# Optimization experiments

Hardware: AMD Instinct MI355X
Metric: run time of the kernel (lower is better)

Reference implementation:

```python
import jax, jax.numpy as jnp
import numpy as np

B, T, F, H, C = 32, 512, 512, 1024, 1000


def setup_inputs() -> dict:
    key = jax.random.key(0)
    ks = jax.random.split(key, 9)
    return {
        "data": jax.random.normal(ks[0], (B, T, F), dtype=jnp.float32),
        "h0": jax.random.normal(ks[1], (H,), dtype=jnp.float32),
        "c0": jax.random.normal(ks[2], (H,), dtype=jnp.float32),
        "w_f": jax.random.normal(ks[3], (H + F, H), dtype=jnp.float32),
        "w_i": jax.random.normal(ks[4], (H + F, H), dtype=jnp.float32),
        "w_c1": jax.random.normal(ks[5], (H + F, H), dtype=jnp.float32),
        "w_o": jax.random.normal(ks[6], (H + F, H), dtype=jnp.float32),
        "fc_w": jax.random.normal(ks[7], (C, H), dtype=jnp.float32),
        "fc_b": jax.random.normal(ks[8], (C,), dtype=jnp.float32),
    }


def reference(data, h0, c0, w_f, w_i, w_c1, w_o, fc_w, fc_b):
    b, t, _ = data.shape
    h = h0.shape[0]
    # Original module never updates h0/c0 inside the time loop, so every
    # timestep sees the same initial state; vectorize gates over time.
    z = jnp.concatenate([jnp.broadcast_to(h0, (b, t, h)), data], axis=-1)  # [B,T,H+F]
    # Stack the 4 gate weights into one fused matmul: [H+F, 4H]
    w_all = jnp.concatenate([w_f, w_i, w_c1, w_o], axis=1)
    g = jnp.einsum('btz,zk->btk', z, w_all)  # [B,T,4H]
    f_g, i_g, c1_g, o_g = jnp.split(g, 4, axis=-1)
    f_g = jax.nn.sigmoid(f_g)
    i_g = jax.nn.sigmoid(i_g)
    c1_g = jnp.tanh(c1_g)
    o_g = jax.nn.sigmoid(o_g)
    c = f_g * c0 + i_g * c1_g          # [B,T,H]
    h_all = o_g * jnp.tanh(c)          # [B,T,H]
    h_last = h_all[:, -1]              # output depends on last timestep only
    logits = jax.nn.relu(h_last @ fc_w.T + fc_b)
    return jax.nn.log_softmax(logits, axis=1)
```

## Files before the change

### kernel.cpp

```cpp
#include <hip/hip_runtime.h>
#include <math.h>

#define BB 32
#define TT 512
#define FF 512
#define HH 1024
#define CC 1000
#define QQ (4*HH)
#define FCB 8
#define KCN 4

template<int JCH, int CHH, int JCD, int CHD>
__global__ __launch_bounds__(512, 4) void k_gates(
    const float* __restrict__ data, const float* __restrict__ h0,
    const float* __restrict__ wf, const float* __restrict__ wi,
    const float* __restrict__ wc, const float* __restrict__ wo,
    float* __restrict__ hp, float* __restrict__ dp)
{
    constexpr int LDSN = (BB*JCD > JCH) ? BB*JCD : JCH;
    __shared__ float lds[LDSN];
    const int t  = threadIdx.x;
    const int bx = blockIdx.x;
    constexpr int NH0 = 2*CHH;

    if (bx < NH0) {
        const int cb2 = bx & 1;
        const int ch  = bx >> 1;
        const int q   = cb2*2048 + t*4;
        const int gate = q >> 10;
        const int k4   = q & (HH-1);
        const float* w = (gate==0) ? wf : (gate==1) ? wi : (gate==2) ? wc : wo;
        if (t < JCH) lds[t] = h0[ch*JCH + t];
        __syncthreads();
        float4 s = make_float4(0.f,0.f,0.f,0.f);
        #pragma unroll
        for (int j = 0; j < JCH; j += 4) {
            const float4 w0 = *(const float4*)(w + (size_t)(ch*JCH + j+0)*HH + k4);
            const float4 w1 = *(const float4*)(w + (size_t)(ch*JCH + j+1)*HH + k4);
            const float4 w2 = *(const float4*)(w + (size_t)(ch*JCH + j+2)*HH + k4);
            const float4 w3 = *(const float4*)(w + (size_t)(ch*JCH + j+3)*HH + k4);
            const float h0v = lds[j+0], h1v = lds[j+1], h2v = lds[j+2], h3v = lds[j+3];
            s.x += h0v*w0.x; s.y += h0v*w0.y; s.z += h0v*w0.z; s.w += h0v*w0.w;
            s.x += h1v*w1.x; s.y += h1v*w1.y; s.z += h1v*w1.z; s.w += h1v*w1.w;
            s.x += h2v*w2.x; s.y += h2v*w2.y; s.z += h2v*w2.z; s.w += h2v*w2.w;
            s.x += h3v*w3.x; s.y += h3v*w3.y; s.z += h3v*w3.z; s.w += h3v*w3.w;
        }
        *(float4*)(hp + (size_t)ch*QQ + q) = s;
    } else {
        const int idx  = bx - NH0;
        const int cb   = idx & 15;
        const int cd   = idx >> 4;
        const int q0   = cb*256;
        const int gate = q0 >> 10;
        const int k0   = q0 & (HH-1);
        const float* w = (gate==0) ? wf : (gate==1) ? wi : (gate==2) ? wc : wo;
        const int jc0  = cd*JCD;

        constexpr int SL = BB*JCD/4;
        for (int s = t; s < SL; s += 512) {
            const int b  = s / (JCD/4);
            const int jj = (s % (JCD/4))*4;
            const float4 v = *(const float4*)(data + (size_t)b*TT*FF + (size_t)(TT-1)*FF + jc0 + jj);
            lds[b*JCD + jj+0] = v.x; lds[b*JCD + jj+1] = v.y;
            lds[b*JCD + jj+2] = v.z; lds[b*JCD + jj+3] = v.w;
        }
        __syncthreads();

        const int c4 = t & 63;
        const int b0 = (t >> 6) * 4;
        const int k4 = k0 + c4*4;
        float4 acc[4];
        #pragma unroll
        for (int bi = 0; bi < 4; ++bi) acc[bi] = make_float4(0.f,0.f,0.f,0.f);

        #pragma unroll 2
        for (int j = 0; j < JCD; j += 4) {
            const float4 w0 = *(const float4*)(w + (size_t)(HH + jc0 + j+0)*HH + k4);
            const float4 w1 = *(const float4*)(w + (size_t)(HH + jc0 + j+1)*HH + k4);
            const float4 w2 = *(const float4*)(w + (size_t)(HH + jc0 + j+2)*HH + k4);
            const float4 w3 = *(const float4*)(w + (size_t)(HH + jc0 + j+3)*HH + k4);
            #pragma unroll
            for (int bi = 0; bi < 4; ++bi) {
                const float d0 = lds[(b0+bi)*JCD + j+0];
                const float d1 = lds[(b0+bi)*JCD + j+1];
                const float d2 = lds[(b0+bi)*JCD + j+2];
                const float d3 = lds[(b0+bi)*JCD + j+3];
                acc[bi].x += d0*w0.x; acc[bi].y += d0*w0.y; acc[bi].z += d0*w0.z; acc[bi].w += d0*w0.w;
                acc[bi].x += d1*w1.x; acc[bi].y += d1*w1.y; acc[bi].z += d1*w1.z; acc[bi].w += d1*w1.w;
                acc[bi].x += d2*w2.x; acc[bi].y += d2*w2.y; acc[bi].z += d2*w2.z; acc[bi].w += d2*w2.w;
                acc[bi].x += d3*w3.x; acc[bi].y += d3*w3.y; acc[bi].z += d3*w3.z; acc[bi].w += d3*w3.w;
            }
        }
        #pragma unroll
        for (int bi = 0; bi < 4; ++bi)
            *(float4*)(dp + ((size_t)cd*BB + b0 + bi)*QQ + q0 + c4*4) = acc[bi];
    }
}

template<int CH, int CD>
__global__ __launch_bounds__(256, 2) void k_cell(
    const float* __restrict__ hp, const float* __restrict__ dp,
    const float* __restrict__ c0, float* __restrict__ hlast)
{
    __shared__ float4 p[4][64];
    const int t    = threadIdx.x;
    const int kblk = blockIdx.x;
    const int b    = blockIdx.y;
    const int g    = t >> 6;
    const int i    = t & 63;
    const int q    = g*HH + kblk*256 + i*4;

    float4 s = make_float4(0.f,0.f,0.f,0.f);
    #pragma unroll 8
    for (int ch = 0; ch < CH; ++ch) {
        const float4 v = *(const float4*)(hp + (size_t)ch*QQ + q);
        s.x += v.x; s.y += v.y; s.z += v.z; s.w += v.w;
    }
    #pragma unroll 8
    for (int cd = 0; cd < CD; ++cd) {
        const float4 v = *(const float4*)(dp + ((size_t)cd*BB + b)*QQ + q);
        s.x += v.x; s.y += v.y; s.z += v.z; s.w += v.w;
    }
    p[g][i] = s;
    __syncthreads();

    if (t < 64) {
        const float4 gf = p[0][t], gi = p[1][t], gc = p[2][t], go = p[3][t];
        const float4 cv = *(const float4*)(c0 + kblk*256 + t*4);
        float4 h;
        {
            const float f = 1.f/(1.f + expf(-gf.x)), ii = 1.f/(1.f + expf(-gi.x));
            const float cg = tanhf(gc.x), o = 1.f/(1.f + expf(-go.x));
            h.x = o*tanhf(f*cv.x + ii*cg);
        }
        {
            const float f = 1.f/(1.f + expf(-gf.y)), ii = 1.f/(1.f + expf(-gi.y));
            const float cg = tanhf(gc.y), o = 1.f/(1.f + expf(-go.y));
            h.y = o*tanhf(f*cv.y + ii*cg);
        }
        {
            const float f = 1.f/(1.f + expf(-gf.z)), ii = 1.f/(1.f + expf(-gi.z));
            const float cg = tanhf(gc.z), o = 1.f/(1.f + expf(-go.z));
            h.z = o*tanhf(f*cv.z + ii*cg);
        }
        {
            const float f = 1.f/(1.f + expf(-gf.w)), ii = 1.f/(1.f + expf(-gi.w));
            const float cg = tanhf(gc.w), o = 1.f/(1.f + expf(-go.w));
            h.w = o*tanhf(f*cv.w + ii*cg);
        }
        *(float4*)(hlast + (size_t)b*HH + kblk*256 + t*4) = h;
    }
}

__global__ __launch_bounds__(256) void k_fc_part(
    const float* __restrict__ hlast, const float* __restrict__ fcw,
    float* __restrict__ pl)
{
    __shared__ float hs[BB][257];
    __shared__ float wl[FCB][257];
    const int t  = threadIdx.x;
    const int c0 = blockIdx.x * FCB;
    const int kc = blockIdx.y;
    const int k0 = kc*256;
    const int b  = t & 31;
    const int cl = t >> 5;
    const int c  = c0 + cl;

    for (int l = t; l < BB*64; l += 256) {
        const int bb = l >> 6, kk = l & 63;
        const float4 v = *(const float4*)(hlast + (size_t)bb*HH + k0 + kk*4);
        hs[bb][kk*4+0] = v.x; hs[bb][kk*4+1] = v.y;
        hs[bb][kk*4+2] = v.z; hs[bb][kk*4+3] = v.w;
    }
    for (int l = t; l < FCB*64; l += 256) {
        const int cc = l >> 6, kk = l & 63;
        const float4 v = *(const float4*)(fcw + (size_t)(c0+cc)*HH + k0 + kk*4);
        wl[cc][kk*4+0] = v.x; wl[cc][kk*4+1] = v.y;
        wl[cc][kk*4+2] = v.z; wl[cc][kk*4+3] = v.w;
    }
    __syncthreads();

    float acc = 0.f;
    #pragma unroll 16
    for (int k = 0; k < 256; ++k)
        acc += hs[b][k] * wl[cl][k];
    pl[((size_t)kc*BB + b)*CC + c] = acc;
}

__global__ __launch_bounds__(256) void k_lsm(
    const float* __restrict__ pl, const float* __restrict__ fcb,
    float* __restrict__ out)
{
    __shared__ float red[8];
    const int b = blockIdx.x, t = threadIdx.x;
    float v[4]; float vmax = -1e30f;
    #pragma unroll
    for (int ci = 0; ci < 4; ++ci) {
        const int c = t + ci*256;
        if (c < CC) {
            float s = pl[((size_t)0*BB + b)*CC + c]
                    + pl[((size_t)1*BB + b)*CC + c]
                    + pl[((size_t)2*BB + b)*CC + c]
                    + pl[((size_t)3*BB + b)*CC + c]
                    + fcb[c];
            v[ci] = fmaxf(s, 0.f);
            vmax = fmaxf(vmax, v[ci]);
        } else v[ci] = -1e30f;
    }
    for (int o = 32; o > 0; o >>= 1) vmax = fmaxf(vmax, __shfl_down(vmax, o, 64));
    const int lane = t & 63, wid = t >> 6;
    if (lane == 0) red[wid] = vmax;
    __syncthreads();
    if (t == 0) red[4] = fmaxf(fmaxf(red[0], red[1]), fmaxf(red[2], red[3]));
    __syncthreads();
    const float m = red[4];
    float se = 0.f;
    #pragma unroll
    for (int ci = 0; ci < 4; ++ci) {
        const int c = t + ci*256;
        if (c < CC) se += expf(v[ci] - m);
    }
    for (int o = 32; o > 0; o >>= 1) se += __shfl_down(se, o, 64);
    if (lane == 0) red[wid] = se;
    __syncthreads();
    if (t == 0) red[5] = m + logf(red[0] + red[1] + red[2] + red[3]);
    __syncthreads();
    const float lse = red[5];
    #pragma unroll
    for (int ci = 0; ci < 4; ++ci) {
        const int c = t + ci*256;
        if (c < CC) out[(size_t)b*CC + c] = v[ci] - lse;
    }
}

extern "C" void kernel_launch(void* const* d_in, const int* in_sizes, int n_in,
                              void* d_out, int out_size, void* d_ws, size_t ws_size,
                              hipStream_t stream) {
    const float* data = (const float*)d_in[0];
    const float* h0   = (const float*)d_in[1];
    const float* c0   = (const float*)d_in[2];
    const float* wf   = (const float*)d_in[3];
    const float* wi   = (const float*)d_in[4];
    const float* wc   = (const float*)d_in[5];
    const float* wo   = (const float*)d_in[6];
    const float* fcw  = (const float*)d_in[7];
    const float* fcb  = (const float*)d_in[8];
    float* out = (float*)d_out;

    const size_t needA = ((size_t)32*QQ + (size_t)16*BB*QQ + (size_t)BB*HH + (size_t)KCN*BB*CC) * 4;
    const bool cfgA = (ws_size >= needA);

    float* ws = (float*)d_ws;
    if (cfgA) {
        float* hp = ws;
        float* dp = hp + (size_t)32*QQ;
        float* hl = dp + (size_t)16*BB*QQ;
        float* pl = hl + (size_t)BB*HH;
        k_gates<32,32,32,16><<<dim3(2*32 + 16*16), 512, 0, stream>>>(data, h0, wf, wi, wc, wo, hp, dp);
        k_cell<32,16><<<dim3(HH/256, BB), 256, 0, stream>>>(hp, dp, c0, hl);
        k_fc_part<<<dim3(CC/FCB, KCN), 256, 0, stream>>>(hl, fcw, pl);
        k_lsm<<<dim3(BB), 256, 0, stream>>>(pl, fcb, out);
    } else {
        float* hp = ws;
        float* dp = hp + (size_t)32*QQ;
        float* hl = dp + (size_t)4*BB*QQ;
        float* pl = hl + (size_t)BB*HH;
        k_gates<32,32,128,4><<<dim3(2*32 + 16*4), 512, 0, stream>>>(data, h0, wf, wi, wc, wo, hp, dp);
        k_cell<32,4><<<dim3(HH/256, BB), 256, 0, stream>>>(hp, dp, c0, hl);
        k_fc_part<<<dim3(CC/FCB, KCN), 256, 0, stream>>>(hl, fcw, pl);
        k_lsm<<<dim3(BB), 256, 0, stream>>>(pl, fcb, out);
    }
}
```

Before: 31.70 us.

## Fuse four LSTM-head kernels into one persistent kernel with grid barriers

```diff
diff --git a/kernel.cpp b/kernel.cpp
--- a/kernel.cpp
+++ b/kernel.cpp
@@ -9,6 +9,247 @@
 #define QQ (4*HH)
 #define FCB 8
 #define KCN 4
+
+#define NBLK 320
+#define PJCH 32
+#define PCHH 32
+#define PJCD 32
+#define PCHD 16
+
+__device__ __forceinline__ void gbar(int* cnt) {
+    __syncthreads();
+    if (threadIdx.x == 0) {
+        __threadfence();
+        atomicAdd(cnt, 1);
+        while (atomicAdd(cnt, 0) < NBLK) __builtin_amdgcn_s_sleep(2);
+        __threadfence();
+    }
+    __syncthreads();
+}
+
+__global__ __launch_bounds__(512, 4) void k_fused(
+    const float* __restrict__ data, const float* __restrict__ h0,
+    const float* __restrict__ c0,
+    const float* __restrict__ wf, const float* __restrict__ wi,
+    const float* __restrict__ wc, const float* __restrict__ wo,
+    const float* __restrict__ fcw, const float* __restrict__ fcb,
+    float* __restrict__ hp, float* __restrict__ dp,
+    float* __restrict__ hl, float* __restrict__ pl,
+    float* __restrict__ out, int* __restrict__ bars)
+{
+    __shared__ __align__(16) float smem[48*257];
+    const int t   = threadIdx.x;
+    const int blk = blockIdx.x;
+
+    if (blk < 2*PCHH) {
+        const int cb2 = blk & 1;
+        const int ch  = blk >> 1;
+        const int q   = cb2*2048 + t*4;
+        const int gate = q >> 10;
+        const int k4   = q & (HH-1);
+        const float* w = (gate==0) ? wf : (gate==1) ? wi : (gate==2) ? wc : wo;
+        if (t < PJCH) smem[t] = h0[ch*PJCH + t];
+        __syncthreads();
+        float4 s = make_float4(0.f,0.f,0.f,0.f);
+        #pragma unroll
+        for (int j = 0; j < PJCH; j += 4) {
+            const float4 w0 = *(const float4*)(w + (size_t)(ch*PJCH + j+0)*HH + k4);
+            const float4 w1 = *(const float4*)(w + (size_t)(ch*PJCH + j+1)*HH + k4);
+            const float4 w2 = *(const float4*)(w + (size_t)(ch*PJCH + j+2)*HH + k4);
+            const float4 w3 = *(const float4*)(w + (size_t)(ch*PJCH + j+3)*HH + k4);
+            const float h0v = smem[j+0], h1v = smem[j+1], h2v = smem[j+2], h3v = smem[j+3];
+            s.x += h0v*w0.x; s.y += h0v*w0.y; s.z += h0v*w0.z; s.w += h0v*w0.w;
+            s.x += h1v*w1.x; s.y += h1v*w1.y; s.z += h1v*w1.z; s.w += h1v*w1.w;
+            s.x += h2v*w2.x; s.y += h2v*w2.y; s.z += h2v*w2.z; s.w += h2v*w2.w;
+            s.x += h3v*w3.x; s.y += h3v*w3.y; s.z += h3v*w3.z; s.w += h3v*w3.w;
+        }
+        *(float4*)(hp + (size_t)ch*QQ + q) = s;
+    } else {
+        const int idx  = blk - 2*PCHH;
+        const int cb   = idx & 15;
+        const int cd   = idx >> 4;
+        const int q0   = cb*256;
+        const int gate = q0 >> 10;
+        const int k0   = q0 & (HH-1);
+        const float* w = (gate==0) ? wf : (gate==1) ? wi : (gate==2) ? wc : wo;
+        const int jc0  = cd*PJCD;
+
+        for (int sl = t; sl < BB*PJCD/4; sl += 512) {
+            const int b  = sl / (PJCD/4);
+            const int jj = (sl % (PJCD/4))*4;
+            const float4 v = *(const float4*)(data + (size_t)b*TT*FF + (size_t)(TT-1)*FF + jc0 + jj);
+            smem[b*PJCD + jj+0] = v.x; smem[b*PJCD + jj+1] = v.y;
+            smem[b*PJCD + jj+2] = v.z; smem[b*PJCD + jj+3] = v.w;
+        }
+        __syncthreads();
+
+        const int c4 = t & 63;
+        const int b0 = (t >> 6) * 4;
+        const int k4 = k0 + c4*4;
+        float4 acc[4];
+        #pragma unroll
+        for (int bi = 0; bi < 4; ++bi) acc[bi] = make_float4(0.f,0.f,0.f,0.f);
+        #pragma unroll 2
+        for (int j = 0; j < PJCD; j += 4) {
+            const float4 w0 = *(const float4*)(w + (size_t)(HH + jc0 + j+0)*HH + k4);
+            const float4 w1 = *(const float4*)(w + (size_t)(HH + jc0 + j+1)*HH + k4);
+            const float4 w2 = *(const float4*)(w + (size_t)(HH + jc0 + j+2)*HH + k4);
+            const float4 w3 = *(const float4*)(w + (size_t)(HH + jc0 + j+3)*HH + k4);
+            #pragma unroll
+            for (int bi = 0; bi < 4; ++bi) {
+                const float d0 = smem[(b0+bi)*PJCD + j+0];
+                const float d1 = smem[(b0+bi)*PJCD + j+1];
+                const float d2 = smem[(b0+bi)*PJCD + j+2];
+                const float d3 = smem[(b0+bi)*PJCD + j+3];
+                acc[bi].x += d0*w0.x; acc[bi].y += d0*w0.y; acc[bi].z += d0*w0.z; acc[bi].w += d0*w0.w;
+                acc[bi].x += d1*w1.x; acc[bi].y += d1*w1.y; acc[bi].z += d1*w1.z; acc[bi].w += d1*w1.w;
+                acc[bi].x += d2*w2.x; acc[bi].y += d2*w2.y; acc[bi].z += d2*w2.z; acc[bi].w += d2*w2.w;
+                acc[bi].x += d3*w3.x; acc[bi].y += d3*w3.y; acc[bi].z += d3*w3.z; acc[bi].w += d3*w3.w;
+            }
+        }
+        #pragma unroll
+        for (int bi = 0; bi < 4; ++bi)
+            *(float4*)(dp + ((size_t)cd*BB + b0 + bi)*QQ + q0 + c4*4) = acc[bi];
+    }
+    gbar(bars + 0);
+
+    if (blk < 64) {
+        float4* p = (float4*)smem;
+        const int sh = t >> 8;
+        const int tt = t & 255;
+        const int unit = blk*2 + sh;
+        const int kblk = unit & 3;
+        const int b    = unit >> 2;
+        const int g = tt >> 6, i = tt & 63;
+        const int q = g*HH + kblk*256 + i*4;
+
+        float4 s = make_float4(0.f,0.f,0.f,0.f);
+        #pragma unroll 8
+        for (int ch = 0; ch < PCHH; ++ch) {
+            const float4 v = *(const float4*)(hp + (size_t)ch*QQ + q);
+            s.x += v.x; s.y += v.y; s.z += v.z; s.w += v.w;
+        }
+        #pragma unroll 8
+        for (int cd = 0; cd < PCHD; ++cd) {
+            const float4 v = *(const float4*)(dp + ((size_t)cd*BB + b)*QQ + q);
+            s.x += v.x; s.y += v.y; s.z += v.z; s.w += v.w;
+        }
+        p[sh*256 + g*64 + i] = s;
+        __syncthreads();
+
+        if (tt < 64) {
+            const float4 gf = p[sh*256 +   0 + tt], gi = p[sh*256 +  64 + tt];
+            const float4 gc = p[sh*256 + 128 + tt], go = p[sh*256 + 192 + tt];
+            const float4 cv = *(const float4*)(c0 + kblk*256 + tt*4);
+            float4 h;
+            {
+                const float f = 1.f/(1.f + expf(-gf.x)), ii = 1.f/(1.f + expf(-gi.x));
+                const float cg = tanhf(gc.x), o = 1.f/(1.f + expf(-go.x));
+                h.x = o*tanhf(f*cv.x + ii*cg);
+            }
+            {
+                const float f = 1.f/(1.f + expf(-gf.y)), ii = 1.f/(1.f + expf(-gi.y));
+                const float cg = tanhf(gc.y), o = 1.f/(1.f + expf(-go.y));
+                h.y = o*tanhf(f*cv.y + ii*cg);
+            }
+            {
+                const float f = 1.f/(1.f + expf(-gf.z)), ii = 1.f/(1.f + expf(-gi.z));
+                const float cg = tanhf(gc.z), o = 1.f/(1.f + expf(-go.z));
+                h.z = o*tanhf(f*cv.z + ii*cg);
+            }
+            {
+                const float f = 1.f/(1.f + expf(-gf.w)), ii = 1.f/(1.f + expf(-gi.w));
+                const float cg = tanhf(gc.w), o = 1.f/(1.f + expf(-go.w));
+                h.w = o*tanhf(f*cv.w + ii*cg);
+            }
+            *(float4*)(hl + (size_t)b*HH + kblk*256 + tt*4) = h;
+        }
+    }
+    gbar(bars + 1);
+
+    if (blk < 252) {
+        float* hs = smem;
+        float* wl = smem + 32*257;
+        const int cxp = blk >> 2;
+        const int kc  = blk & 3;
+        const int cb0 = cxp*16;
+        const int k0  = kc*256;
+
+        for (int l = t; l < 32*64; l += 512) {
+            const int bb = l >> 6, kk = l & 63;
+            const float4 v = *(const float4*)(hl + (size_t)bb*HH + k0 + kk*4);
+            hs[bb*257 + kk*4+0] = v.x; hs[bb*257 + kk*4+1] = v.y;
+            hs[bb*257 + kk*4+2] = v.z; hs[bb*257 + kk*4+3] = v.w;
+        }
+        for (int l = t; l < 16*64; l += 512) {
+            const int cc = l >> 6, kk = l & 63;
+            if (cb0 + cc < CC) {
+                const float4 v = *(const float4*)(fcw + (size_t)(cb0+cc)*HH + k0 + kk*4);
+                wl[cc*257 + kk*4+0] = v.x; wl[cc*257 + kk*4+1] = v.y;
+                wl[cc*257 + kk*4+2] = v.z; wl[cc*257 + kk*4+3] = v.w;
+            }
+        }
+        __syncthreads();
+
+        const int b  = t & 31;
+        const int cl = t >> 5;
+        const int c  = cb0 + cl;
+        float acc = 0.f;
+        #pragma unroll 16
+        for (int k = 0; k < 256; ++k)
+            acc += hs[b*257 + k] * wl[cl*257 + k];
+        if (c < CC) pl[((size_t)kc*BB + b)*CC + c] = acc;
+    }
+    gbar(bars + 2);
+
+    if (blk < 16) {
+        float* red = smem;
+        const int sh = t >> 8;
+        const int tt = t & 255;
+        const int b  = blk*2 + sh;
+        float v[4]; float vmax = -1e30f;
+        #pragma unroll
+        for (int ci = 0; ci < 4; ++ci) {
+            const int c = tt + ci*256;
+            if (c < CC) {
+                float s = pl[((size_t)0*BB + b)*CC + c]
+                        + pl[((size_t)1*BB + b)*CC + c]
+                        + pl[((size_t)2*BB + b)*CC + c]
+                        + pl[((size_t)3*BB + b)*CC + c]
+                        + fcb[c];
+                v[ci] = fmaxf(s, 0.f);
+                vmax = fmaxf(vmax, v[ci]);
+            } else v[ci] = -1e30f;
+        }
+        for (int o = 32; o > 0; o >>= 1) vmax = fmaxf(vmax, __shfl_down(vmax, o, 64));
+        const int lane = tt & 63, wid = tt >> 6;
+        if (lane == 0) red[sh*10 + wid] = vmax;
+        __syncthreads();
+        if (tt == 0)
+            red[sh*10 + 8] = fmaxf(fmaxf(red[sh*10+0], red[sh*10+1]),
+                                   fmaxf(red[sh*10+2], red[sh*10+3]));
+        __syncthreads();
+        const float m = red[sh*10 + 8];
+        float se = 0.f;
+        #pragma unroll
+        for (int ci = 0; ci < 4; ++ci) {
+            const int c = tt + ci*256;
+            if (c < CC) se += expf(v[ci] - m);
+        }
+        for (int o = 32; o > 0; o >>= 1) se += __shfl_down(se, o, 64);
+        if (lane == 0) red[sh*10 + wid] = se;
+        __syncthreads();
+        if (tt == 0)
+            red[sh*10 + 9] = m + logf(red[sh*10+0] + red[sh*10+1] + red[sh*10+2] + red[sh*10+3]);
+        __syncthreads();
+        const float lse = red[sh*10 + 9];
+        #pragma unroll
+        for (int ci = 0; ci < 4; ++ci) {
+            const int c = tt + ci*256;
+            if (c < CC) out[(size_t)b*CC + c] = v[ci] - lse;
+        }
+    }
+}
 
 template<int JCH, int CHH, int JCD, int CHD>
 __global__ __launch_bounds__(512, 4) void k_gates(
@@ -22,73 +263,47 @@
     const int t  = threadIdx.x;
     const int bx = blockIdx.x;
     constexpr int NH0 = 2*CHH;
-
     if (bx < NH0) {
-        const int cb2 = bx & 1;
-        const int ch  = bx >> 1;
-        const int q   = cb2*2048 + t*4;
-        const int gate = q >> 10;
-        const int k4   = q & (HH-1);
+        const int cb2 = bx & 1, ch = bx >> 1;
+        const int q = cb2*2048 + t*4;
+        const int gate = q >> 10, k4 = q & (HH-1);
         const float* w = (gate==0) ? wf : (gate==1) ? wi : (gate==2) ? wc : wo;
         if (t < JCH) lds[t] = h0[ch*JCH + t];
         __syncthreads();
         float4 s = make_float4(0.f,0.f,0.f,0.f);
         #pragma unroll
-        for (int j = 0; j < JCH; j += 4) {
-            const float4 w0 = *(const float4*)(w + (size_t)(ch*JCH + j+0)*HH + k4);
-            const float4 w1 = *(const float4*)(w + (size_t)(ch*JCH + j+1)*HH + k4);
-            const float4 w2 = *(const float4*)(w + (size_t)(ch*JCH + j+2)*HH + k4);
-            const float4 w3 = *(const float4*)(w + (size_t)(ch*JCH + j+3)*HH + k4);
-            const float h0v = lds[j+0], h1v = lds[j+1], h2v = lds[j+2], h3v = lds[j+3];
-            s.x += h0v*w0.x; s.y += h0v*w0.y; s.z += h0v*w0.z; s.w += h0v*w0.w;
-            s.x += h1v*w1.x; s.y += h1v*w1.y; s.z += h1v*w1.z; s.w += h1v*w1.w;
-            s.x += h2v*w2.x; s.y += h2v*w2.y; s.z += h2v*w2.z; s.w += h2v*w2.w;
-            s.x += h3v*w3.x; s.y += h3v*w3.y; s.z += h3v*w3.z; s.w += h3v*w3.w;
+        for (int j = 0; j < JCH; ++j) {
+            const float4 wv = *(const float4*)(w + (size_t)(ch*JCH + j)*HH + k4);
+            const float hv = lds[j];
+            s.x += hv*wv.x; s.y += hv*wv.y; s.z += hv*wv.z; s.w += hv*wv.w;
         }
         *(float4*)(hp + (size_t)ch*QQ + q) = s;
     } else {
-        const int idx  = bx - NH0;
-        const int cb   = idx & 15;
-        const int cd   = idx >> 4;
-        const int q0   = cb*256;
-        const int gate = q0 >> 10;
-        const int k0   = q0 & (HH-1);
+        const int idx = bx - NH0;
+        const int cb = idx & 15, cd = idx >> 4;
+        const int q0 = cb*256;
+        const int gate = q0 >> 10, k0 = q0 & (HH-1);
         const float* w = (gate==0) ? wf : (gate==1) ? wi : (gate==2) ? wc : wo;
-        const int jc0  = cd*JCD;
-
-        constexpr int SL = BB*JCD/4;
-        for (int s = t; s < SL; s += 512) {
-            const int b  = s / (JCD/4);
-            const int jj = (s % (JCD/4))*4;
+        const int jc0 = cd*JCD;
+        for (int s = t; s < BB*JCD/4; s += 512) {
+            const int b = s / (JCD/4), jj = (s % (JCD/4))*4;
             const float4 v = *(const float4*)(data + (size_t)b*TT*FF + (size_t)(TT-1)*FF + jc0 + jj);
             lds[b*JCD + jj+0] = v.x; lds[b*JCD + jj+1] = v.y;
             lds[b*JCD + jj+2] = v.z; lds[b*JCD + jj+3] = v.w;
         }
         __syncthreads();
-
-        const int c4 = t & 63;
-        const int b0 = (t >> 6) * 4;
+        const int c4 = t & 63, b0 = (t >> 6)*4;
         const int k4 = k0 + c4*4;
         float4 acc[4];
         #pragma unroll
         for (int bi = 0; bi < 4; ++bi) acc[bi] = make_float4(0.f,0.f,0.f,0.f);
-
-        #pragma unroll 2
-        for (int j = 0; j < JCD; j += 4) {
-            const float4 w0 = *(const float4*)(w + (size_t)(HH + jc0 + j+0)*HH + k4);
-            const float4 w1 = *(const float4*)(w + (size_t)(HH + jc0 + j+1)*HH + k4);
-            const float4 w2 = *(const float4*)(w + (size_t)(HH + jc0 + j+2)*HH + k4);
-            const float4 w3 = *(const float4*)(w + (size_t)(HH + jc0 + j+3)*HH + k4);
+        for (int j = 0; j < JCD; ++j) {
+            const float4 wv = *(const float4*)(w + (size_t)(HH + jc0 + j)*HH + k4);
             #pragma unroll
             for (int bi = 0; bi < 4; ++bi) {
-                const float d0 = lds[(b0+bi)*JCD + j+0];
-                const float d1 = lds[(b0+bi)*JCD + j+1];
-                const float d2 = lds[(b0+bi)*JCD + j+2];
-                const float d3 = lds[(b0+bi)*JCD + j+3];
-                acc[bi].x += d0*w0.x; acc[bi].y += d0*w0.y; acc[bi].z += d0*w0.z; acc[bi].w += d0*w0.w;
-                acc[bi].x += d1*w1.x; acc[bi].y += d1*w1.y; acc[bi].z += d1*w1.z; acc[bi].w += d1*w1.w;
-                acc[bi].x += d2*w2.x; acc[bi].y += d2*w2.y; acc[bi].z += d2*w2.z; acc[bi].w += d2*w2.w;
-                acc[bi].x += d3*w3.x; acc[bi].y += d3*w3.y; acc[bi].z += d3*w3.z; acc[bi].w += d3*w3.w;
+                const float dv = lds[(b0+bi)*JCD + j];
+                acc[bi].x += dv*wv.x; acc[bi].y += dv*wv.y;
+                acc[bi].z += dv*wv.z; acc[bi].w += dv*wv.w;
             }
         }
         #pragma unroll
@@ -103,13 +318,9 @@
     const float* __restrict__ c0, float* __restrict__ hlast)
 {
     __shared__ float4 p[4][64];
-    const int t    = threadIdx.x;
-    const int kblk = blockIdx.x;
-    const int b    = blockIdx.y;
-    const int g    = t >> 6;
-    const int i    = t & 63;
-    const int q    = g*HH + kblk*256 + i*4;
-
+    const int t = threadIdx.x, kblk = blockIdx.x, b = blockIdx.y;
+    const int g = t >> 6, i = t & 63;
+    const int q = g*HH + kblk*256 + i*4;
     float4 s = make_float4(0.f,0.f,0.f,0.f);
     #pragma unroll 8
     for (int ch = 0; ch < CH; ++ch) {
@@ -123,31 +334,14 @@
     }
     p[g][i] = s;
     __syncthreads();
-
     if (t < 64) {
         const float4 gf = p[0][t], gi = p[1][t], gc = p[2][t], go = p[3][t];
         const float4 cv = *(const float4*)(c0 + kblk*256 + t*4);
         float4 h;
-        {
-            const float f = 1.f/(1.f + expf(-gf.x)), ii = 1.f/(1.f + expf(-gi.x));
-            const float cg = tanhf(gc.x), o = 1.f/(1.f + expf(-go.x));
-            h.x = o*tanhf(f*cv.x + ii*cg);
-        }
-        {
-            const float f = 1.f/(1.f + expf(-gf.y)), ii = 1.f/(1.f + expf(-gi.y));
-            const float cg = tanhf(gc.y), o = 1.f/(1.f + expf(-go.y));
-            h.y = o*tanhf(f*cv.y + ii*cg);
-        }
-        {
-            const float f = 1.f/(1.f + expf(-gf.z)), ii = 1.f/(1.f + expf(-gi.z));
-            const float cg = tanhf(gc.z), o = 1.f/(1.f + expf(-go.z));
-            h.z = o*tanhf(f*cv.z + ii*cg);
-        }
-        {
-            const float f = 1.f/(1.f + expf(-gf.w)), ii = 1.f/(1.f + expf(-gi.w));
-            const float cg = tanhf(gc.w), o = 1.f/(1.f + expf(-go.w));
-            h.w = o*tanhf(f*cv.w + ii*cg);
-        }
+        { const float f=1.f/(1.f+expf(-gf.x)), ii=1.f/(1.f+expf(-gi.x)), cg=tanhf(gc.x), o=1.f/(1.f+expf(-go.x)); h.x=o*tanhf(f*cv.x+ii*cg); }
+        { const float f=1.f/(1.f+expf(-gf.y)), ii=1.f/(1.f+expf(-gi.y)), cg=tanhf(gc.y), o=1.f/(1.f+expf(-go.y)); h.y=o*tanhf(f*cv.y+ii*cg); }
+        { const float f=1.f/(1.f+expf(-gf.z)), ii=1.f/(1.f+expf(-gi.z)), cg=tanhf(gc.z), o=1.f/(1.f+expf(-go.z)); h.z=o*tanhf(f*cv.z+ii*cg); }
+        { const float f=1.f/(1.f+expf(-gf.w)), ii=1.f/(1.f+expf(-gi.w)), cg=tanhf(gc.w), o=1.f/(1.f+expf(-go.w)); h.w=o*tanhf(f*cv.w+ii*cg); }
         *(float4*)(hlast + (size_t)b*HH + kblk*256 + t*4) = h;
     }
 }
@@ -158,14 +352,12 @@
 {
     __shared__ float hs[BB][257];
     __shared__ float wl[FCB][257];
-    const int t  = threadIdx.x;
+    const int t = threadIdx.x;
     const int c0 = blockIdx.x * FCB;
     const int kc = blockIdx.y;
     const int k0 = kc*256;
-    const int b  = t & 31;
-    const int cl = t >> 5;
-    const int c  = c0 + cl;
-
+    const int b = t & 31, cl = t >> 5;
+    const int c = c0 + cl;
     for (int l = t; l < BB*64; l += 256) {
         const int bb = l >> 6, kk = l & 63;
         const float4 v = *(const float4*)(hlast + (size_t)bb*HH + k0 + kk*4);
@@ -179,11 +371,9 @@
         wl[cc][kk*4+2] = v.z; wl[cc][kk*4+3] = v.w;
     }
     __syncthreads();
-
     float acc = 0.f;
     #pragma unroll 16
-    for (int k = 0; k < 256; ++k)
-        acc += hs[b][k] * wl[cl][k];
+    for (int k = 0; k < 256; ++k) acc += hs[b][k] * wl[cl][k];
     pl[((size_t)kc*BB + b)*CC + c] = acc;
 }
 
@@ -198,11 +388,8 @@
     for (int ci = 0; ci < 4; ++ci) {
         const int c = t + ci*256;
         if (c < CC) {
-            float s = pl[((size_t)0*BB + b)*CC + c]
-                    + pl[((size_t)1*BB + b)*CC + c]
-                    + pl[((size_t)2*BB + b)*CC + c]
-                    + pl[((size_t)3*BB + b)*CC + c]
-                    + fcb[c];
+            float s = pl[((size_t)0*BB + b)*CC + c] + pl[((size_t)1*BB + b)*CC + c]
+                    + pl[((size_t)2*BB + b)*CC + c] + pl[((size_t)3*BB + b)*CC + c] + fcb[c];
             v[ci] = fmaxf(s, 0.f);
             vmax = fmaxf(vmax, v[ci]);
         } else v[ci] = -1e30f;
@@ -247,27 +434,26 @@
     const float* fcb  = (const float*)d_in[8];
     float* out = (float*)d_out;
 
-    const size_t needA = ((size_t)32*QQ + (size_t)16*BB*QQ + (size_t)BB*HH + (size_t)KCN*BB*CC) * 4;
-    const bool cfgA = (ws_size >= needA);
-
-    float* ws = (float*)d_ws;
-    if (cfgA) {
-        float* hp = ws;
-        float* dp = hp + (size_t)32*QQ;
-        float* hl = dp + (size_t)16*BB*QQ;
-        float* pl = hl + (size_t)BB*HH;
-        k_gates<32,32,32,16><<<dim3(2*32 + 16*16), 512, 0, stream>>>(data, h0, wf, wi, wc, wo, hp, dp);
-        k_cell<32,16><<<dim3(HH/256, BB), 256, 0, stream>>>(hp, dp, c0, hl);
-        k_fc_part<<<dim3(CC/FCB, KCN), 256, 0, stream>>>(hl, fcw, pl);
-        k_lsm<<<dim3(BB), 256, 0, stream>>>(pl, fcb, out);
+    int*   bars = (int*)d_ws;
+    float* hp = (float*)d_ws + 16;
+    float* dp = hp + (size_t)PCHH*QQ;
+    float* hl = dp + (size_t)PCHD*BB*QQ;
+    float* pl = hl + (size_t)BB*HH;
+    const size_t need = (16 + (size_t)PCHH*QQ + (size_t)PCHD*BB*QQ
+                         + (size_t)BB*HH + (size_t)KCN*BB*CC) * 4;
+
+    if (ws_size >= need) {
+        hipMemsetAsync(bars, 0, 16, stream);
+        k_fused<<<dim3(NBLK), 512, 0, stream>>>(data, h0, c0, wf, wi, wc, wo,
+                                                fcw, fcb, hp, dp, hl, pl, out, bars);
     } else {
-        float* hp = ws;
-        float* dp = hp + (size_t)32*QQ;
-        float* hl = dp + (size_t)4*BB*QQ;
-        float* pl = hl + (size_t)BB*HH;
-        k_gates<32,32,128,4><<<dim3(2*32 + 16*4), 512, 0, stream>>>(data, h0, wf, wi, wc, wo, hp, dp);
-        k_cell<32,4><<<dim3(HH/256, BB), 256, 0, stream>>>(hp, dp, c0, hl);
-        k_fc_part<<<dim3(CC/FCB, KCN), 256, 0, stream>>>(hl, fcw, pl);
-        k_lsm<<<dim3(BB), 256, 0, stream>>>(pl, fcb, out);
-    }
-}
+        float* hpB = (float*)d_ws;
+        float* dpB = hpB + (size_t)32*QQ;
+        float* hlB = dpB + (size_t)4*BB*QQ;
+        float* plB = hlB + (size_t)BB*HH;
+        k_gates<32,32,128,4><<<dim3(2*32 + 16*4), 512, 0, stream>>>(data, h0, wf, wi, wc, wo, hpB, dpB);
+        k_cell<32,4><<<dim3(HH/256, BB), 256, 0, stream>>>(hpB, dpB, c0, hlB);
+        k_fc_part<<<dim3(CC/FCB, KCN), 256, 0, stream>>>(hlB, fcw, plB);
+        k_lsm<<<dim3(BB), 256, 0, stream>>>(plB, fcb, out);
+    }
+}
```

Result: slower. 123.4 us (+289.4%).

## Fuse FC and log-softmax into one kernel using a last-block ticket

Applied to the files above, without the earlier changes.

```diff
diff --git a/kernel.cpp b/kernel.cpp
--- a/kernel.cpp
+++ b/kernel.cpp
@@ -8,7 +8,6 @@
 #define CC 1000
 #define QQ (4*HH)
 #define FCB 8
-#define KCN 4
 
 template<int JCH, int CHH, int JCD, int CHD>
 __global__ __launch_bounds__(512, 4) void k_gates(
@@ -56,8 +55,7 @@
         const float* w = (gate==0) ? wf : (gate==1) ? wi : (gate==2) ? wc : wo;
         const int jc0  = cd*JCD;
 
-        constexpr int SL = BB*JCD/4;
-        for (int s = t; s < SL; s += 512) {
+        for (int s = t; s < BB*JCD/4; s += 512) {
             const int b  = s / (JCD/4);
             const int jj = (s % (JCD/4))*4;
             const float4 v = *(const float4*)(data + (size_t)b*TT*FF + (size_t)(TT-1)*FF + jc0 + jj);
@@ -100,15 +98,16 @@
 template<int CH, int CD>
 __global__ __launch_bounds__(256, 2) void k_cell(
     const float* __restrict__ hp, const float* __restrict__ dp,
-    const float* __restrict__ c0, float* __restrict__ hlast)
+    const float* __restrict__ c0, float* __restrict__ hlast,
+    int* __restrict__ ticket)
 {
     __shared__ float4 p[4][64];
     const int t    = threadIdx.x;
     const int kblk = blockIdx.x;
     const int b    = blockIdx.y;
-    const int g    = t >> 6;
-    const int i    = t & 63;
-    const int q    = g*HH + kblk*256 + i*4;
+    if (kblk == 0 && b == 0 && t == 0) atomicExch(ticket, 0);
+    const int g = t >> 6, i = t & 63;
+    const int q = g*HH + kblk*256 + i*4;
 
     float4 s = make_float4(0.f,0.f,0.f,0.f);
     #pragma unroll 8
@@ -128,108 +127,81 @@
         const float4 gf = p[0][t], gi = p[1][t], gc = p[2][t], go = p[3][t];
         const float4 cv = *(const float4*)(c0 + kblk*256 + t*4);
         float4 h;
-        {
-            const float f = 1.f/(1.f + expf(-gf.x)), ii = 1.f/(1.f + expf(-gi.x));
-            const float cg = tanhf(gc.x), o = 1.f/(1.f + expf(-go.x));
-            h.x = o*tanhf(f*cv.x + ii*cg);
-        }
-        {
-            const float f = 1.f/(1.f + expf(-gf.y)), ii = 1.f/(1.f + expf(-gi.y));
-            const float cg = tanhf(gc.y), o = 1.f/(1.f + expf(-go.y));
-            h.y = o*tanhf(f*cv.y + ii*cg);
-        }
-        {
-            const float f = 1.f/(1.f + expf(-gf.z)), ii = 1.f/(1.f + expf(-gi.z));
-            const float cg = tanhf(gc.z), o = 1.f/(1.f + expf(-go.z));
-            h.z = o*tanhf(f*cv.z + ii*cg);
-        }
-        {
-            const float f = 1.f/(1.f + expf(-gf.w)), ii = 1.f/(1.f + expf(-gi.w));
-            const float cg = tanhf(gc.w), o = 1.f/(1.f + expf(-go.w));
-            h.w = o*tanhf(f*cv.w + ii*cg);
-        }
+        { const float f=1.f/(1.f+expf(-gf.x)), ii=1.f/(1.f+expf(-gi.x)), cg=tanhf(gc.x), o=1.f/(1.f+expf(-go.x)); h.x=o*tanhf(f*cv.x+ii*cg); }
+        { const float f=1.f/(1.f+expf(-gf.y)), ii=1.f/(1.f+expf(-gi.y)), cg=tanhf(gc.y), o=1.f/(1.f+expf(-go.y)); h.y=o*tanhf(f*cv.y+ii*cg); }
+        { const float f=1.f/(1.f+expf(-gf.z)), ii=1.f/(1.f+expf(-gi.z)), cg=tanhf(gc.z), o=1.f/(1.f+expf(-go.z)); h.z=o*tanhf(f*cv.z+ii*cg); }
+        { const float f=1.f/(1.f+expf(-gf.w)), ii=1.f/(1.f+expf(-gi.w)), cg=tanhf(gc.w), o=1.f/(1.f+expf(-go.w)); h.w=o*tanhf(f*cv.w+ii*cg); }
         *(float4*)(hlast + (size_t)b*HH + kblk*256 + t*4) = h;
     }
 }
 
-__global__ __launch_bounds__(256) void k_fc_part(
+__global__ __launch_bounds__(256) void k_fc_tail(
     const float* __restrict__ hlast, const float* __restrict__ fcw,
-    float* __restrict__ pl)
+    const float* __restrict__ fcb, float* __restrict__ out,
+    int* __restrict__ ticket)
 {
     __shared__ float hs[BB][257];
     __shared__ float wl[FCB][257];
+    __shared__ int lastFlag;
     const int t  = threadIdx.x;
     const int c0 = blockIdx.x * FCB;
-    const int kc = blockIdx.y;
-    const int k0 = kc*256;
     const int b  = t & 31;
     const int cl = t >> 5;
     const int c  = c0 + cl;
-
-    for (int l = t; l < BB*64; l += 256) {
-        const int bb = l >> 6, kk = l & 63;
-        const float4 v = *(const float4*)(hlast + (size_t)bb*HH + k0 + kk*4);
-        hs[bb][kk*4+0] = v.x; hs[bb][kk*4+1] = v.y;
-        hs[bb][kk*4+2] = v.z; hs[bb][kk*4+3] = v.w;
-    }
-    for (int l = t; l < FCB*64; l += 256) {
-        const int cc = l >> 6, kk = l & 63;
-        const float4 v = *(const float4*)(fcw + (size_t)(c0+cc)*HH + k0 + kk*4);
-        wl[cc][kk*4+0] = v.x; wl[cc][kk*4+1] = v.y;
-        wl[cc][kk*4+2] = v.z; wl[cc][kk*4+3] = v.w;
-    }
+    float acc = 0.f;
+    #pragma unroll
+    for (int kc = 0; kc < HH/256; ++kc) {
+        const int k0 = kc*256;
+        for (int l = t; l < BB*64; l += 256) {
+            const int bb = l >> 6, kk = l & 63;
+            const float4 v = *(const float4*)(hlast + (size_t)bb*HH + k0 + kk*4);
+            hs[bb][kk*4+0] = v.x; hs[bb][kk*4+1] = v.y;
+            hs[bb][kk*4+2] = v.z; hs[bb][kk*4+3] = v.w;
+        }
+        for (int l = t; l < FCB*64; l += 256) {
+            const int cc = l >> 6, kk = l & 63;
+            const float4 v = *(const float4*)(fcw + (size_t)(c0+cc)*HH + k0 + kk*4);
+            wl[cc][kk*4+0] = v.x; wl[cc][kk*4+1] = v.y;
+            wl[cc][kk*4+2] = v.z; wl[cc][kk*4+3] = v.w;
+        }
+        __syncthreads();
+        #pragma unroll 16
+        for (int k = 0; k < 256; ++k)
+            acc += hs[b][k] * wl[cl][k];
+        __syncthreads();
+    }
+    out[(size_t)b*CC + c] = fmaxf(acc + fcb[c], 0.f);
+
     __syncthreads();
-
-    float acc = 0.f;
-    #pragma unroll 16
-    for (int k = 0; k < 256; ++k)
-        acc += hs[b][k] * wl[cl][k];
-    pl[((size_t)kc*BB + b)*CC + c] = acc;
-}
-
-__global__ __launch_bounds__(256) void k_lsm(
-    const float* __restrict__ pl, const float* __restrict__ fcb,
-    float* __restrict__ out)
-{
-    __shared__ float red[8];
-    const int b = blockIdx.x, t = threadIdx.x;
-    float v[4]; float vmax = -1e30f;
-    #pragma unroll
-    for (int ci = 0; ci < 4; ++ci) {
-        const int c = t + ci*256;
-        if (c < CC) {
-            float s = pl[((size_t)0*BB + b)*CC + c]
-                    + pl[((size_t)1*BB + b)*CC + c]
-                    + pl[((size_t)2*BB + b)*CC + c]
-                    + pl[((size_t)3*BB + b)*CC + c]
-                    + fcb[c];
-            v[ci] = fmaxf(s, 0.f);
-            vmax = fmaxf(vmax, v[ci]);
-        } else v[ci] = -1e30f;
-    }
-    for (int o = 32; o > 0; o >>= 1) vmax = fmaxf(vmax, __shfl_down(vmax, o, 64));
-    const int lane = t & 63, wid = t >> 6;
-    if (lane == 0) red[wid] = vmax;
+    if (t == 0) {
+        __threadfence();
+        lastFlag = (atomicAdd(ticket, 1) == (int)gridDim.x - 1);
+    }
     __syncthreads();
-    if (t == 0) red[4] = fmaxf(fmaxf(red[0], red[1]), fmaxf(red[2], red[3]));
-    __syncthreads();
-    const float m = red[4];
+    if (!lastFlag) return;
+    __threadfence();
+
+    const int rb = t >> 3;
+    const int l8 = t & 7;
+    float vm = -1e30f;
+    #pragma unroll 8
+    for (int i = 0; i < 125; ++i)
+        vm = fmaxf(vm, out[(size_t)rb*CC + l8 + i*8]);
+    vm = fmaxf(vm, __shfl_xor(vm, 1, 64));
+    vm = fmaxf(vm, __shfl_xor(vm, 2, 64));
+    vm = fmaxf(vm, __shfl_xor(vm, 4, 64));
     float se = 0.f;
-    #pragma unroll
-    for (int ci = 0; ci < 4; ++ci) {
-        const int c = t + ci*256;
-        if (c < CC) se += expf(v[ci] - m);
-    }
-    for (int o = 32; o > 0; o >>= 1) se += __shfl_down(se, o, 64);
-    if (lane == 0) red[wid] = se;
-    __syncthreads();
-    if (t == 0) red[5] = m + logf(red[0] + red[1] + red[2] + red[3]);
-    __syncthreads();
-    const float lse = red[5];
-    #pragma unroll
-    for (int ci = 0; ci < 4; ++ci) {
-        const int c = t + ci*256;
-        if (c < CC) out[(size_t)b*CC + c] = v[ci] - lse;
+    #pragma unroll 8
+    for (int i = 0; i < 125; ++i)
+        se += expf(out[(size_t)rb*CC + l8 + i*8] - vm);
+    se += __shfl_xor(se, 1, 64);
+    se += __shfl_xor(se, 2, 64);
+    se += __shfl_xor(se, 4, 64);
+    const float lse = vm + logf(se);
+    #pragma unroll 8
+    for (int i = 0; i < 125; ++i) {
+        const size_t idx = (size_t)rb*CC + l8 + i*8;
+        out[idx] = out[idx] - lse;
     }
 }
 
@@ -247,27 +219,24 @@
     const float* fcb  = (const float*)d_in[8];
     float* out = (float*)d_out;
 
-    const size_t needA = ((size_t)32*QQ + (size_t)16*BB*QQ + (size_t)BB*HH + (size_t)KCN*BB*CC) * 4;
+    int*   tk = (int*)d_ws;
+    float* base = (float*)d_ws + 16;
+    const size_t needA = (16 + (size_t)32*QQ + (size_t)16*BB*QQ + (size_t)BB*HH) * 4;
     const bool cfgA = (ws_size >= needA);
 
-    float* ws = (float*)d_ws;
     if (cfgA) {
-        float* hp = ws;
+        float* hp = base;
         float* dp = hp + (size_t)32*QQ;
         float* hl = dp + (size_t)16*BB*QQ;
-        float* pl = hl + (size_t)BB*HH;
         k_gates<32,32,32,16><<<dim3(2*32 + 16*16), 512, 0, stream>>>(data, h0, wf, wi, wc, wo, hp, dp);
-        k_cell<32,16><<<dim3(HH/256, BB), 256, 0, stream>>>(hp, dp, c0, hl);
-        k_fc_part<<<dim3(CC/FCB, KCN), 256, 0, stream>>>(hl, fcw, pl);
-        k_lsm<<<dim3(BB), 256, 0, stream>>>(pl, fcb, out);
+        k_cell<32,16><<<dim3(HH/256, BB), 256, 0, stream>>>(hp, dp, c0, hl, tk);
+        k_fc_tail<<<dim3(CC/FCB), 256, 0, stream>>>(hl, fcw, fcb, out, tk);
     } else {
-        float* hp = ws;
+        float* hp = base;
         float* dp = hp + (size_t)32*QQ;
         float* hl = dp + (size_t)4*BB*QQ;
-        float* pl = hl + (size_t)BB*HH;
         k_gates<32,32,128,4><<<dim3(2*32 + 16*4), 512, 0, stream>>>(data, h0, wf, wi, wc, wo, hp, dp);
-        k_cell<32,4><<<dim3(HH/256, BB), 256, 0, stream>>>(hp, dp, c0, hl);
-        k_fc_part<<<dim3(CC/FCB, KCN), 256, 0, stream>>>(hl, fcw, pl);
-        k_lsm<<<dim3(BB), 256, 0, stream>>>(pl, fcb, out);
-    }
-}
+        k_cell<32,4><<<dim3(HH/256, BB), 256, 0, stream>>>(hp, dp, c0, hl, tk);
+        k_fc_tail<<<dim3(CC/FCB), 256, 0, stream>>>(hl, fcw, fcb, out, tk);
+    }
+}
```

Result: slower. 83.82 us (+164.4%).
